# Optimization experiments

Measured on AMD Instinct MI355X. Metric: run time of the kernel, lower is better.

The kernel has to match this reference:

```python
import jax, jax.numpy as jnp
import numpy as np

N_NODES = 100000
N_EDGES = 1600000
EMBED_DIM = 64
NUM_HEADS = 4
HEAD_DIM = EMBED_DIM // NUM_HEADS  # 16


def mish(x):
    return x * jnp.tanh(jax.nn.softplus(x))


def setup_inputs() -> dict:
    key = jax.random.key(0)
    ks = jax.random.split(key, 8)
    x = jax.random.normal(ks[0], (N_NODES, EMBED_DIM), dtype=jnp.float32)
    senders = jax.random.randint(ks[1], (N_EDGES,), 0, N_NODES, dtype=jnp.int32)
    receivers = jax.random.randint(ks[2], (N_EDGES,), 0, N_NODES, dtype=jnp.int32)
    sc = 1.0 / np.sqrt(EMBED_DIM)
    # DenseGeneral(features=(H, d)) for senders / receivers, with bias
    Ws = jax.random.normal(ks[3], (EMBED_DIM, NUM_HEADS, HEAD_DIM), dtype=jnp.float32) * sc
    bs = jnp.zeros((NUM_HEADS, HEAD_DIM), dtype=jnp.float32)
    Wr = jax.random.normal(ks[4], (EMBED_DIM, NUM_HEADS, HEAD_DIM), dtype=jnp.float32) * sc
    br = jnp.zeros((NUM_HEADS, HEAD_DIM), dtype=jnp.float32)
    # Dense(1) on last axis (head_dim), weights shared across heads
    aw = jax.random.normal(ks[5], (HEAD_DIM,), dtype=jnp.float32) * (1.0 / np.sqrt(HEAD_DIM))
    ab = jnp.zeros((1,), dtype=jnp.float32)
    return {"x": x, "Ws": Ws, "bs": bs, "Wr": Wr, "br": br,
            "aw": aw, "ab": ab, "senders": senders, "receivers": receivers}


def reference(x, Ws, bs, Wr, br, aw, ab, senders, receivers):
    n = x.shape[0]
    # Node-level projections (same math as per-edge DenseGeneral, less traffic)
    s_proj = jnp.einsum('nf,fhd->nhd', x, Ws) + bs  # [N,H,d]
    r_proj = jnp.einsum('nf,fhd->nhd', x, Wr) + br  # [N,H,d]
    se = s_proj[senders]      # [E,H,d] gather of sender features
    re = r_proj[receivers]    # [E,H,d] gather of receiver features
    # GATv2 logit: Dense(1)(mish(s + r)) -> [E,H]
    logits = jnp.einsum('ehd,d->eh', mish(se + re), aw) + ab[0]
    # Segment softmax over incoming edges of each receiver node
    lmax = jax.ops.segment_max(logits, receivers, num_segments=n)
    ex = jnp.exp(logits - lmax[receivers])
    denom = jax.ops.segment_sum(ex, receivers, num_segments=n)
    alpha = ex / denom[receivers]  # [E,H]
    # Scatter-sum weighted sender features back to receiver nodes
    out = jax.ops.segment_sum(alpha[..., None] * se, receivers, num_segments=n)  # [N,H,d]
    return out.reshape(n, -1)  # [N, H*d]
```

## Files before the change

### kernel.cpp

```cpp
#include <hip/hip_runtime.h>
#include <hip/hip_fp16.h>
#include <math.h>

#define N_NODES 100000
#define N_EDGES 1600000
#define EMBED 64
#define HEADS 4
#define HDIM 16

#define SLOTS 64

#define BKT_SHIFT 8
#define BKT_NODES 256
#define NBKT 391
#define BKT_CAP 5120
#define TILE 4096
#define NTILE 391
#define NGRP (N_EDGES / 4)

#define NODES_BLK 64
#define NBLK_PROJ 1563
#define SMEM_BYTES 52224

#define LOG2E 1.44269504f

__device__ __forceinline__ float mish_aw(float z, float awc) {
    float ex  = __expf(fminf(z, 30.f));
    float u   = 1.f + ex;
    float den = fmaf(u, u, 1.f);
    float f   = fmaf(-2.f, __builtin_amdgcn_rcpf(den), 1.f);
    return z * awc * f;
}

template<int CTRL>
__device__ __forceinline__ float ror_add(float t) {
    int x = __builtin_amdgcn_mov_dpp(__float_as_int(t), CTRL, 0xF, 0xF, true);
    return t + __int_as_float(x);
}
__device__ __forceinline__ float head_reduce(float t) {
    t = ror_add<0x121>(t);
    t = ror_add<0x122>(t);
    t = ror_add<0x124>(t);
    t = ror_add<0x128>(t);
    return t;
}

template<int CTRL>
__device__ __forceinline__ __half2 hror_add(__half2 t) {
    int x = __builtin_amdgcn_mov_dpp(__builtin_bit_cast(int, t), CTRL, 0xF, 0xF, true);
    return __hadd2(t, __builtin_bit_cast(__half2, x));
}
__device__ __forceinline__ __half2 head_reduce_h2(__half2 t) {
    t = hror_add<0x121>(t);
    t = hror_add<0x122>(t);
    t = hror_add<0x124>(t);
    t = hror_add<0x128>(t);
    return t;
}

__global__ __launch_bounds__(256) void proj_bucketa_kernel(
        const float* __restrict__ x,
        const float* __restrict__ Ws, const float* __restrict__ bs,
        const float* __restrict__ Wr, const float* __restrict__ br,
        const int* __restrict__ senders, const int* __restrict__ receivers,
        unsigned short* __restrict__ sph, unsigned short* __restrict__ rph,
        int* __restrict__ bktcnt, int* __restrict__ bkt) {
    __shared__ __align__(16) char smem[SMEM_BYTES];
    int tid = threadIdx.x;
    if (blockIdx.x < NBLK_PROJ) {
        float* wsT = (float*)smem;
        float* wrT = wsT + 64 * 68;
        float* xsh = wrT + 64 * 68;
        for (int i = tid; i < 4096; i += 256) {
            int k = i >> 6, o = i & 63;
            wsT[o * 68 + k] = Ws[i];
            wrT[o * 68 + k] = Wr[i];
        }
        int nb = blockIdx.x * NODES_BLK;
        for (int i = 0; i < 4; ++i) {
            int g = i * 256 + tid;
            int nl = g >> 4;
            int k4 = g & 15;
            if (nb + nl < N_NODES) {
                float4 v = ((const float4*)(x + ((size_t)(nb + nl) << 6)))[k4];
                *(float4*)(xsh + nl * 68 + (k4 << 2)) = v;
            }
        }
        __syncthreads();
        int o = tid & 63;
        int w = tid >> 6;
        float bsv = bs[o], brv = br[o];
        float accs[16], accr[16];
#pragma unroll
        for (int p = 0; p < 16; ++p) { accs[p] = bsv; accr[p] = brv; }
        const float4* ws4 = (const float4*)wsT + o * 17;
        const float4* wr4 = (const float4*)wrT + o * 17;
        const float4* xs4 = (const float4*)xsh + (w << 4) * 17;
#pragma unroll 4
        for (int k4 = 0; k4 < 16; ++k4) {
            float4 a = ws4[k4];
            float4 b = wr4[k4];
#pragma unroll
            for (int p = 0; p < 16; ++p) {
                float4 xv = xs4[p * 17 + k4];
                accs[p] += xv.x * a.x + xv.y * a.y + xv.z * a.z + xv.w * a.w;
                accr[p] += xv.x * b.x + xv.y * b.y + xv.z * b.z + xv.w * b.w;
            }
        }
        int node0 = nb + (w << 4);
#pragma unroll
        for (int p = 0; p < 16; ++p) {
            int node = node0 + p;
            if (node < N_NODES) {
                sph[(node << 6) + o] = __half_as_ushort(__float2half_rn(accs[p]));
                rph[(node << 6) + o] = __half_as_ushort(__float2half_rn(accr[p]));
            }
        }
    } else {
        int* hist = (int*)smem;
        int* base = hist + NBKT;
        int* cur  = base + NBKT;
        for (int i = tid; i < NBKT; i += 256) hist[i] = 0;
        __syncthreads();
        int g0 = (blockIdx.x - NBLK_PROJ) * (TILE / 4);
        int4 r[4], s[4];
        bool v[4];
#pragma unroll
        for (int t = 0; t < 4; ++t) {
            int g = g0 + t * 256 + tid;
            v[t] = (g < NGRP);
            if (v[t]) {
                r[t] = ((const int4*)receivers)[g];
                s[t] = ((const int4*)senders)[g];
                atomicAdd(&hist[r[t].x >> BKT_SHIFT], 1);
                atomicAdd(&hist[r[t].y >> BKT_SHIFT], 1);
                atomicAdd(&hist[r[t].z >> BKT_SHIFT], 1);
                atomicAdd(&hist[r[t].w >> BKT_SHIFT], 1);
            }
        }
        __syncthreads();
        for (int i = tid; i < NBKT; i += 256) {
            int h = hist[i];
            base[i] = (h > 0) ? atomicAdd(&bktcnt[i], h) : 0;
            cur[i] = 0;
        }
        __syncthreads();
#pragma unroll
        for (int t = 0; t < 4; ++t) {
            if (v[t]) {
                int b, rk, slot;
                b = r[t].x >> BKT_SHIFT; rk = atomicAdd(&cur[b], 1); slot = base[b] + rk;
                if (slot < BKT_CAP) bkt[b * BKT_CAP + slot] = ((r[t].x & (BKT_NODES - 1)) << 17) | s[t].x;
                b = r[t].y >> BKT_SHIFT; rk = atomicAdd(&cur[b], 1); slot = base[b] + rk;
                if (slot < BKT_CAP) bkt[b * BKT_CAP + slot] = ((r[t].y & (BKT_NODES - 1)) << 17) | s[t].y;
                b = r[t].z >> BKT_SHIFT; rk = atomicAdd(&cur[b], 1); slot = base[b] + rk;
                if (slot < BKT_CAP) bkt[b * BKT_CAP + slot] = ((r[t].z & (BKT_NODES - 1)) << 17) | s[t].z;
                b = r[t].w >> BKT_SHIFT; rk = atomicAdd(&cur[b], 1); slot = base[b] + rk;
                if (slot < BKT_CAP) bkt[b * BKT_CAP + slot] = ((r[t].w & (BKT_NODES - 1)) << 17) | s[t].w;
            }
        }
    }
}

__global__ __launch_bounds__(1024) void bucketb_kernel(
        const int* __restrict__ bktcnt, const int* __restrict__ bkt,
        int* __restrict__ cursor, int* __restrict__ csr) {
    __shared__ int lcur[BKT_NODES];
    int tid = threadIdx.x;
    int b = blockIdx.x;
    if (tid < BKT_NODES) lcur[tid] = 0;
    __syncthreads();
    int cnt = bktcnt[b];
    if (cnt > BKT_CAP) cnt = BKT_CAP;
    const int* bb = bkt + b * BKT_CAP;
    for (int i = tid; i < cnt; i += 1024) {
        int vv = bb[i];
        int rl = vv >> 17;
        int sv = vv & 0x1FFFF;
        int slot = atomicAdd(&lcur[rl], 1);
        if (slot < SLOTS) csr[((((b << BKT_SHIFT) + rl)) << 6) + slot] = sv << 7;
    }
    __syncthreads();
    if (tid < BKT_NODES) {
        int node = (b << BKT_SHIFT) + tid;
        if (node < N_NODES) cursor[node] = lcur[tid];
    }
}

__global__ __launch_bounds__(256) void fused_gather_kernel(
                                    const unsigned short* __restrict__ sph,
                                    const unsigned short* __restrict__ rph,
                                    const int* __restrict__ csr,
                                    const int* __restrict__ cursor,
                                    const float* __restrict__ aw,
                                    const float* __restrict__ ab,
                                    float* __restrict__ out) {
    int wave = (blockIdx.x * blockDim.x + threadIdx.x) >> 6;
    wave = __builtin_amdgcn_readfirstlane(wave);
    int lane = threadIdx.x & 63;
    int deg = cursor[wave];
    deg = (deg > SLOTS) ? SLOTS : deg;
    const int* cbase = csr + (wave << 6);
    const char* splb = (const char*)sph + (lane << 1);
    float rp  = __half2float(__ushort_as_half(rph[(wave << 6) + lane]));
    float awc = aw[lane & 15];
    float abl = ab[0] * LOG2E;
    __half2 k_pk    = __float2half2_rn(0.5f * LOG2E);
    __half2 rpk_pk  = __float2half2_rn(rp * 0.5f * LOG2E);
    __half2 aw_pk   = __float2half2_rn(awc);
    __half2 rpa_pk  = __float2half2_rn(rp * awc);
    __half2 ones    = __float2half2_rn(1.0f);
    __half2 neg2    = __float2half2_rn(-2.0f);
    float l = 0.f, acc = 0.f;
    int i = 0;
    for (; i + 8 <= deg; i += 8) {
        unsigned short su[8];
#pragma unroll
        for (int j = 0; j < 8; ++j) su[j] = *(const unsigned short*)(splb + cbase[i + j]);
#pragma unroll
        for (int j = 0; j < 4; ++j) {
            __half2 sp  = __halves2half2(__ushort_as_half(su[2 * j]),
                                         __ushort_as_half(su[2 * j + 1]));
            __half2 arg = __hfma2(sp, k_pk, rpk_pk);
            __half2 t2  = h2exp2(arg);
            __half2 w   = __hmul2(t2, t2);
            __half2 u   = __hadd2(w, ones);
            __half2 den = __hfma2(u, u, ones);
            __half2 r   = h2rcp(den);
            __half2 f   = __hfma2(neg2, r, ones);
            __half2 za  = __hfma2(sp, aw_pk, rpa_pk);
            __half2 tt  = head_reduce_h2(__hmul2(za, f));
            float p0 = __builtin_amdgcn_exp2f(fmaf(__low2float(tt),  LOG2E, abl));
            float p1 = __builtin_amdgcn_exp2f(fmaf(__high2float(tt), LOG2E, abl));
            l += p0 + p1;
            acc = fmaf(p0, __low2float(sp), fmaf(p1, __high2float(sp), acc));
        }
    }
    for (; i + 2 <= deg; i += 2) {
        __half2 sp  = __halves2half2(__ushort_as_half(*(const unsigned short*)(splb + cbase[i])),
                                     __ushort_as_half(*(const unsigned short*)(splb + cbase[i + 1])));
        __half2 arg = __hfma2(sp, k_pk, rpk_pk);
        __half2 t2  = h2exp2(arg);
        __half2 w   = __hmul2(t2, t2);
        __half2 u   = __hadd2(w, ones);
        __half2 den = __hfma2(u, u, ones);
        __half2 r   = h2rcp(den);
        __half2 f   = __hfma2(neg2, r, ones);
        __half2 za  = __hfma2(sp, aw_pk, rpa_pk);
        __half2 tt  = head_reduce_h2(__hmul2(za, f));
        float p0 = __builtin_amdgcn_exp2f(fmaf(__low2float(tt),  LOG2E, abl));
        float p1 = __builtin_amdgcn_exp2f(fmaf(__high2float(tt), LOG2E, abl));
        l += p0 + p1;
        acc = fmaf(p0, __low2float(sp), fmaf(p1, __high2float(sp), acc));
    }
    if (i < deg) {
        float sp0 = __half2float(__ushort_as_half(*(const unsigned short*)(splb + cbase[i])));
        float t0 = head_reduce(mish_aw(sp0 + rp, awc));
        float p = __builtin_amdgcn_exp2f(fmaf(t0, LOG2E, abl));
        l += p;
        acc = fmaf(p, sp0, acc);
    }
    out[(wave << 6) + lane] = (deg > 0) ? acc * __builtin_amdgcn_rcpf(l) : 0.f;
}

extern "C" void kernel_launch(void* const* d_in, const int* in_sizes, int n_in,
                              void* d_out, int out_size, void* d_ws, size_t ws_size,
                              hipStream_t stream) {
    const float* x  = (const float*)d_in[0];
    const float* Ws = (const float*)d_in[1];
    const float* bs = (const float*)d_in[2];
    const float* Wr = (const float*)d_in[3];
    const float* br = (const float*)d_in[4];
    const float* aw = (const float*)d_in[5];
    const float* ab = (const float*)d_in[6];
    const int* senders   = (const int*)d_in[7];
    const int* receivers = (const int*)d_in[8];
    float* out = (float*)d_out;

    char* wsp = (char*)d_ws;
    unsigned short* sph = (unsigned short*)wsp;  wsp += (size_t)N_NODES * EMBED * 2;
    unsigned short* rph = (unsigned short*)wsp;  wsp += (size_t)N_NODES * EMBED * 2;
    int* csr    = (int*)wsp;  wsp += (size_t)N_NODES * SLOTS * 4;
    int* cursor = (int*)wsp;  wsp += (size_t)N_NODES * 4;
    int* bkt    = (int*)wsp;  wsp += (size_t)NBKT * BKT_CAP * 4;
    int* bktcnt = (int*)wsp;  wsp += 512 * 4;

    hipMemsetAsync(bktcnt, 0, NBKT * 4, stream);

    proj_bucketa_kernel<<<NBLK_PROJ + NTILE, 256, 0, stream>>>(
        x, Ws, bs, Wr, br, senders, receivers, sph, rph, bktcnt, bkt);

    bucketb_kernel<<<NBKT, 1024, 0, stream>>>(bktcnt, bkt, cursor, csr);

    int gather_blocks = (N_NODES * 64 + 255) / 256;
    fused_gather_kernel<<<gather_blocks, 256, 0, stream>>>(sph, rph, csr, cursor,
                                                           aw, ab, out);
}
```

Baseline: 128.3 us.

## Fuse bucket-to-CSR pass into gather kernel using LDS-resident CSR

Merges the second bucketing pass and the attention gather into one kernel. Each block builds a per-bucket CSR of 128 nodes in shared memory and then processes those nodes directly, with lanes broadcasting neighbor offsets through readlane. This drops one kernel launch and the global CSR and cursor write-then-read round trip. Buckets shrink to 128 nodes so the CSR fits in LDS. The cost is fewer, larger blocks (782 blocks of 512 threads, each wave handling 16 nodes serially), which may hurt load balance and occupancy given the 32KB LDS per block. The unchanged projection/bucketing kernel must also be correct with the new bucket constants, which cannot be checked here.

Result: slower. 155.2 us (+21.0%).

```diff
diff --git a/kernel.cpp b/kernel.cpp
--- a/kernel.cpp
+++ b/kernel.cpp
@@ -10,10 +10,10 @@
 
 #define SLOTS 64
 
-#define BKT_SHIFT 8
-#define BKT_NODES 256
-#define NBKT 391
-#define BKT_CAP 5120
+#define BKT_SHIFT 7
+#define BKT_NODES 128
+#define NBKT 782
+#define BKT_CAP 2816
 #define TILE 4096
 #define NTILE 391
 #define NGRP (N_EDGES / 4)
@@ -162,9 +162,13 @@
     }
 }
 
-__global__ __launch_bounds__(1024) void bucketb_kernel(
+__global__ __launch_bounds__(512) void bucket_gather_kernel(
+        const unsigned short* __restrict__ sph,
+        const unsigned short* __restrict__ rph,
         const int* __restrict__ bktcnt, const int* __restrict__ bkt,
-        int* __restrict__ cursor, int* __restrict__ csr) {
+        const float* __restrict__ aw, const float* __restrict__ ab,
+        float* __restrict__ out) {
+    __shared__ int csr_lds[BKT_NODES * SLOTS];
     __shared__ int lcur[BKT_NODES];
     int tid = threadIdx.x;
     int b = blockIdx.x;
@@ -173,58 +177,73 @@
     int cnt = bktcnt[b];
     if (cnt > BKT_CAP) cnt = BKT_CAP;
     const int* bb = bkt + b * BKT_CAP;
-    for (int i = tid; i < cnt; i += 1024) {
+    for (int i = tid; i < cnt; i += 512) {
         int vv = bb[i];
         int rl = vv >> 17;
         int sv = vv & 0x1FFFF;
         int slot = atomicAdd(&lcur[rl], 1);
-        if (slot < SLOTS) csr[((((b << BKT_SHIFT) + rl)) << 6) + slot] = sv << 7;
+        if (slot < SLOTS) csr_lds[(rl << 6) + slot] = sv << 7;
     }
     __syncthreads();
-    if (tid < BKT_NODES) {
-        int node = (b << BKT_SHIFT) + tid;
-        if (node < N_NODES) cursor[node] = lcur[tid];
-    }
-}
-
-__global__ __launch_bounds__(256) void fused_gather_kernel(
-                                    const unsigned short* __restrict__ sph,
-                                    const unsigned short* __restrict__ rph,
-                                    const int* __restrict__ csr,
-                                    const int* __restrict__ cursor,
-                                    const float* __restrict__ aw,
-                                    const float* __restrict__ ab,
-                                    float* __restrict__ out) {
-    int wave = (blockIdx.x * blockDim.x + threadIdx.x) >> 6;
-    wave = __builtin_amdgcn_readfirstlane(wave);
-    int lane = threadIdx.x & 63;
-    int deg = cursor[wave];
-    deg = (deg > SLOTS) ? SLOTS : deg;
-    const int* cbase = csr + (wave << 6);
+
+    int lane = tid & 63;
+    int w = tid >> 6;
+    int nbase = b << BKT_SHIFT;
     const char* splb = (const char*)sph + (lane << 1);
-    float rp  = __half2float(__ushort_as_half(rph[(wave << 6) + lane]));
     float awc = aw[lane & 15];
     float abl = ab[0] * LOG2E;
-    __half2 k_pk    = __float2half2_rn(0.5f * LOG2E);
-    __half2 rpk_pk  = __float2half2_rn(rp * 0.5f * LOG2E);
-    __half2 aw_pk   = __float2half2_rn(awc);
-    __half2 rpa_pk  = __float2half2_rn(rp * awc);
-    __half2 ones    = __float2half2_rn(1.0f);
-    __half2 neg2    = __float2half2_rn(-2.0f);
-    float l = 0.f, acc = 0.f;
-    int i = 0;
-    for (; i + 8 <= deg; i += 8) {
-        unsigned short su[8];
-#pragma unroll
-        for (int j = 0; j < 8; ++j) su[j] = *(const unsigned short*)(splb + cbase[i + j]);
-#pragma unroll
-        for (int j = 0; j < 4; ++j) {
-            __half2 sp  = __halves2half2(__ushort_as_half(su[2 * j]),
-                                         __ushort_as_half(su[2 * j + 1]));
+    __half2 k_pk  = __float2half2_rn(0.5f * LOG2E);
+    __half2 aw_pk = __float2half2_rn(awc);
+    __half2 ones  = __float2half2_rn(1.0f);
+    __half2 neg2  = __float2half2_rn(-2.0f);
+
+    for (int t = 0; t < 16; ++t) {
+        int nl = (w << 4) + t;
+        int node = nbase + nl;
+        if (node >= N_NODES) break;
+        int deg = __builtin_amdgcn_readfirstlane(lcur[nl]);
+        deg = (deg > SLOTS) ? SLOTS : deg;
+        int myoff = csr_lds[(nl << 6) + lane];
+        float rp  = __half2float(__ushort_as_half(rph[(node << 6) + lane]));
+        __half2 rpk_pk = __float2half2_rn(rp * 0.5f * LOG2E);
+        __half2 rpa_pk = __float2half2_rn(rp * awc);
+        float l = 0.f, acc = 0.f;
+        int i = 0;
+        for (; i + 8 <= deg; i += 8) {
+            int o_[8];
+            unsigned short su[8];
+#pragma unroll
+            for (int j = 0; j < 8; ++j) o_[j] = __builtin_amdgcn_readlane(myoff, i + j);
+#pragma unroll
+            for (int j = 0; j < 8; ++j) su[j] = *(const unsigned short*)(splb + o_[j]);
+#pragma unroll
+            for (int j = 0; j < 4; ++j) {
+                __half2 sp  = __halves2half2(__ushort_as_half(su[2 * j]),
+                                             __ushort_as_half(su[2 * j + 1]));
+                __half2 arg = __hfma2(sp, k_pk, rpk_pk);
+                __half2 t2  = h2exp2(arg);
+                __half2 wv  = __hmul2(t2, t2);
+                __half2 u   = __hadd2(wv, ones);
+                __half2 den = __hfma2(u, u, ones);
+                __half2 r   = h2rcp(den);
+                __half2 f   = __hfma2(neg2, r, ones);
+                __half2 za  = __hfma2(sp, aw_pk, rpa_pk);
+                __half2 tt  = head_reduce_h2(__hmul2(za, f));
+                float p0 = __builtin_amdgcn_exp2f(fmaf(__low2float(tt),  LOG2E, abl));
+                float p1 = __builtin_amdgcn_exp2f(fmaf(__high2float(tt), LOG2E, abl));
+                l += p0 + p1;
+                acc = fmaf(p0, __low2float(sp), fmaf(p1, __high2float(sp), acc));
+            }
+        }
+        for (; i + 2 <= deg; i += 2) {
+            int o0 = __builtin_amdgcn_readlane(myoff, i);
+            int o1 = __builtin_amdgcn_readlane(myoff, i + 1);
+            __half2 sp  = __halves2half2(__ushort_as_half(*(const unsigned short*)(splb + o0)),
+                                         __ushort_as_half(*(const unsigned short*)(splb + o1)));
             __half2 arg = __hfma2(sp, k_pk, rpk_pk);
             __half2 t2  = h2exp2(arg);
-            __half2 w   = __hmul2(t2, t2);
-            __half2 u   = __hadd2(w, ones);
+            __half2 wv  = __hmul2(t2, t2);
+            __half2 u   = __hadd2(wv, ones);
             __half2 den = __hfma2(u, u, ones);
             __half2 r   = h2rcp(den);
             __half2 f   = __hfma2(neg2, r, ones);
@@ -235,32 +254,16 @@
             l += p0 + p1;
             acc = fmaf(p0, __low2float(sp), fmaf(p1, __high2float(sp), acc));
         }
+        if (i < deg) {
+            int o0 = __builtin_amdgcn_readlane(myoff, i);
+            float sp0 = __half2float(__ushort_as_half(*(const unsigned short*)(splb + o0)));
+            float t0 = head_reduce(mish_aw(sp0 + rp, awc));
+            float p = __builtin_amdgcn_exp2f(fmaf(t0, LOG2E, abl));
+            l += p;
+            acc = fmaf(p, sp0, acc);
+        }
+        out[(node << 6) + lane] = (deg > 0) ? acc * __builtin_amdgcn_rcpf(l) : 0.f;
     }
-    for (; i + 2 <= deg; i += 2) {
-        __half2 sp  = __halves2half2(__ushort_as_half(*(const unsigned short*)(splb + cbase[i])),
-                                     __ushort_as_half(*(const unsigned short*)(splb + cbase[i + 1])));
-        __half2 arg = __hfma2(sp, k_pk, rpk_pk);
-        __half2 t2  = h2exp2(arg);
-        __half2 w   = __hmul2(t2, t2);
-        __half2 u   = __hadd2(w, ones);
-        __half2 den = __hfma2(u, u, ones);
-        __half2 r   = h2rcp(den);
-        __half2 f   = __hfma2(neg2, r, ones);
-        __half2 za  = __hfma2(sp, aw_pk, rpa_pk);
-        __half2 tt  = head_reduce_h2(__hmul2(za, f));
-        float p0 = __builtin_amdgcn_exp2f(fmaf(__low2float(tt),  LOG2E, abl));
-        float p1 = __builtin_amdgcn_exp2f(fmaf(__high2float(tt), LOG2E, abl));
-        l += p0 + p1;
-        acc = fmaf(p0, __low2float(sp), fmaf(p1, __high2float(sp), acc));
-    }
-    if (i < deg) {
-        float sp0 = __half2float(__ushort_as_half(*(const unsigned short*)(splb + cbase[i])));
-        float t0 = head_reduce(mish_aw(sp0 + rp, awc));
-        float p = __builtin_amdgcn_exp2f(fmaf(t0, LOG2E, abl));
-        l += p;
-        acc = fmaf(p, sp0, acc);
-    }
-    out[(wave << 6) + lane] = (deg > 0) ? acc * __builtin_amdgcn_rcpf(l) : 0.f;
 }
 
 extern "C" void kernel_launch(void* const* d_in, const int* in_sizes, int n_in,
@@ -280,19 +283,13 @@
     char* wsp = (char*)d_ws;
     unsigned short* sph = (unsigned short*)wsp;  wsp += (size_t)N_NODES * EMBED * 2;
     unsigned short* rph = (unsigned short*)wsp;  wsp += (size_t)N_NODES * EMBED * 2;
-    int* csr    = (int*)wsp;  wsp += (size_t)N_NODES * SLOTS * 4;
-    int* cursor = (int*)wsp;  wsp += (size_t)N_NODES * 4;
     int* bkt    = (int*)wsp;  wsp += (size_t)NBKT * BKT_CAP * 4;
-    int* bktcnt = (int*)wsp;  wsp += 512 * 4;
+    int* bktcnt = (int*)wsp;  wsp += 1024 * 4;
 
     hipMemsetAsync(bktcnt, 0, NBKT * 4, stream);
 
     proj_bucketa_kernel<<<NBLK_PROJ + NTILE, 256, 0, stream>>>(
         x, Ws, bs, Wr, br, senders, receivers, sph, rph, bktcnt, bkt);
 
-    bucketb_kernel<<<NBKT, 1024, 0, stream>>>(bktcnt, bkt, cursor, csr);
-
-    int gather_blocks = (N_NODES * 64 + 255) / 256;
-    fused_gather_kernel<<<gather_blocks, 256, 0, stream>>>(sph, rph, csr, cursor,
-                                                           aw, ab, out);
-}
+    bucket_gather_kernel<<<NBKT, 512, 0, stream>>>(sph, rph, bktcnt, bkt, aw, ab, out);
+}
```
